# Optimization experiments

Measured on AMD Instinct MI355X. Metric: run time of the kernel, lower is better.

Reference implementation:

```python
import jax, jax.numpy as jnp
import numpy as np

C, H, W, NC, LC = 512, 160, 160, 1203, 64


def setup_inputs() -> dict:
    key = jax.random.key(0)
    ks = jax.random.split(key, 8)
    return {
        "cls_feat": jax.random.normal(ks[0], (1, C, H, W), jnp.float32),
        "loc_feat": jax.random.normal(ks[1], (1, LC, H, W), jnp.float32),
        "conf": jax.random.uniform(ks[2], (1,), jnp.float32, 0.2, 0.8),
        "pf_w": jax.random.normal(ks[3], (C,), jnp.float32) * 0.02,   # pf 1x1 conv, C->1
        "pf_b": jnp.zeros((1,), jnp.float32),
        "vocab_w": jax.random.normal(ks[4], (NC, C), jnp.float32) * 0.02,  # conv2linear weight
        "vocab_b": jnp.zeros((NC,), jnp.float32),
        "loc_w": jax.random.normal(ks[5], (LC, LC), jnp.float32) * 0.02,   # loc 1x1 conv
        "loc_b": jnp.zeros((LC,), jnp.float32),
    }


def reference(cls_feat, loc_feat, conf, pf_w, pf_b, vocab_w, vocab_b, loc_w, loc_b):
    B, Cc, Hh, Ww = cls_feat.shape
    # proposal-filter score: 1x1 conv C->1 on batch 0, flattened to [HW]
    pf_score = jnp.einsum('c,chw->hw', pf_w, cls_feat[0]).reshape(-1) + pf_b  # [HW]
    mask = jax.nn.sigmoid(pf_score) > conf[0]  # [HW] bool
    # tokens: [1, HW, C]
    tok = cls_feat.reshape(B, Cc, Hh * Ww).transpose(0, 2, 1)
    # static-shape equivalent of the proposal filter: zero masked-out tokens
    tok = tok * mask[None, :, None].astype(tok.dtype)
    # vocab linear (converted 1x1 conv): [1, HW, NC] -> [1, NC, HW]
    cls_out = (jnp.einsum('bnc,vc->bnv', tok, vocab_w) + vocab_b).transpose(0, 2, 1)
    # localization 1x1 conv
    loc_out = jnp.einsum('oi,bihw->bohw', loc_w, loc_feat) + loc_b[None, :, None, None]
    return loc_out, cls_out, mask
```

## Files before the change

### kernel.cpp

```cpp
#include <hip/hip_runtime.h>
#include <math.h>


constexpr int C_   = 512;
constexpr int HW_  = 25600;
constexpr int NC_  = 1203;
constexpr int VPAD_ = 1216;

constexpr int LOC_OFF_  = 0;
constexpr int CLS_OFF_  = 64 * HW_;
constexpr int MASK_OFF_ = CLS_OFF_ + NC_ * HW_;

constexpr int PF_BLOCKS_    = HW_ / 64;
constexpr int LOC_BLOCKS_   = 400;
constexpr int FILL_BLOCKS_  = 2048;
constexpr int TRANS_BLOCKS_ = 19 * 8;

typedef float vfloat4 __attribute__((ext_vector_type(4)));

__global__ void k_init(int* cnt) { *cnt = 0; }

__global__ __launch_bounds__(256) void k_main(
    const float* __restrict__ cls_feat, const float* __restrict__ loc_feat,
    const float* __restrict__ conf, const float* __restrict__ pf_w,
    const float* __restrict__ pf_b, const float* __restrict__ vocab_w,
    const float* __restrict__ vocab_b, const float* __restrict__ loc_w,
    const float* __restrict__ loc_b, float* __restrict__ out,
    int* __restrict__ cnt, int* __restrict__ idxList,
    float* __restrict__ AT4, int jcap)
{
    const int bid = blockIdx.x;
    const int tid = threadIdx.x;

    if (bid < PF_BLOCKS_) {
        __shared__ double sPart[256];
        const int hwi   = tid & 63;
        const int slice = tid >> 6;
        const int hw    = bid * 64 + hwi;
        const float* p  = cls_feat + (size_t)slice * 128 * HW_ + hw;
        const float* w  = pf_w + slice * 128;
        double acc = 0.0;
        #pragma unroll 4
        for (int k = 0; k < 128; ++k)
            acc += (double)w[k] * (double)p[(size_t)k * HW_];
        sPart[tid] = acc;
        __syncthreads();
        if (slice == 0) {
            double s = sPart[hwi] + sPart[64 + hwi] + sPart[128 + hwi] +
                       sPart[192 + hwi] + (double)pf_b[0];
            double sig = 1.0 / (1.0 + exp(-s));
            bool m = sig > (double)conf[0];
            out[MASK_OFF_ + hw] = m ? 1.0f : 0.0f;
            if (m) {
                int pos = atomicAdd(cnt, 1);
                if (pos < HW_) idxList[pos] = hw;
            }
        }
    } else if (bid < PF_BLOCKS_ + LOC_BLOCKS_) {
        const int j   = bid - PF_BLOCKS_;
        const int hwb = j % 100;
        const int o0  = (j / 100) * 16;
        __shared__ float sw[16][64];
        for (int i = tid; i < 16 * 64; i += 256)
            sw[i >> 6][i & 63] = loc_w[(o0 + (i >> 6)) * 64 + (i & 63)];
        __syncthreads();
        const int hw = hwb * 256 + tid;
        float acc[16];
        #pragma unroll
        for (int r = 0; r < 16; ++r) acc[r] = loc_b[o0 + r];
        for (int i = 0; i < 64; ++i) {
            float f = loc_feat[(size_t)i * HW_ + hw];
            #pragma unroll
            for (int r = 0; r < 16; ++r) acc[r] += sw[r][i] * f;
        }
        #pragma unroll
        for (int r = 0; r < 16; ++r)
            out[LOC_OFF_ + (size_t)(o0 + r) * HW_ + hw] = acc[r];
    } else if (bid < PF_BLOCKS_ + LOC_BLOCKS_ + FILL_BLOCKS_) {
        const int fb = bid - PF_BLOCKS_ - LOC_BLOCKS_;
        const int total4 = NC_ * HW_ / 4;
        vfloat4* o = (vfloat4*)(out + CLS_OFF_);
        for (int i = fb * 256 + tid; i < total4; i += FILL_BLOCKS_ * 256) {
            int v = i / (HW_ / 4);
            float b = vocab_b[v];
            vfloat4 val = {b, b, b, b};
            __builtin_nontemporal_store(val, &o[i]);
        }
    } else {
        if (jcap <= 0) return;
        const int tb = bid - PF_BLOCKS_ - LOC_BLOCKS_ - FILL_BLOCKS_;
        const int v0 = (tb % 19) * 64;
        const int k0 = (tb / 19) * 64;
        __shared__ float t[64][65];
        const int c  = tid & 63;
        const int r4 = tid >> 6;
        #pragma unroll
        for (int i = 0; i < 16; ++i) {
            const int r = r4 * 16 + i;
            const int v = v0 + r;
            t[r][c] = (v < NC_) ? vocab_w[(size_t)v * C_ + k0 + c] : 0.f;
        }
        __syncthreads();
        #pragma unroll
        for (int i = 0; i < 16; ++i) {
            const int k = r4 * 16 + i;
            const int kg = k0 + k;
            AT4[((size_t)(kg >> 2) * VPAD_ + v0 + c) * 4 + (kg & 3)] = t[c][k];
        }
    }
}

__global__ __launch_bounds__(256) void k_gatherJ(
    const float* __restrict__ cls_feat, const int* __restrict__ cnt,
    const int* __restrict__ idxList, float* __restrict__ BdT, int jcap)
{
    const int count = min(*cnt, HW_);
    if (count > jcap) return;
    const int t = threadIdx.x;
    for (int j = blockIdx.x; j < count; j += gridDim.x) {
        const int hw = idxList[j];
        BdT[(size_t)j * C_ + t]       = cls_feat[(size_t)t * HW_ + hw];
        BdT[(size_t)j * C_ + 256 + t] = cls_feat[(size_t)(256 + t) * HW_ + hw];
    }
}

__global__ __launch_bounds__(256) void k_gemm4(
    const float* __restrict__ AT4, const float* __restrict__ vocab_b,
    const int* __restrict__ cnt, const int* __restrict__ idxList,
    const float* __restrict__ BdT, float* __restrict__ out, int jcap)
{
    const int count = min(*cnt, HW_);
    if (count == 0 || count > jcap) return;

    const int tid  = threadIdx.x;
    const int lane = tid & 63;
    const int w    = tid >> 6;
    const int v0   = blockIdx.x * 64;
    const int v    = v0 + lane;
    const float* __restrict__ Acol = AT4 + (size_t)(v0 + lane) * 4;

    for (int j4 = blockIdx.y * 4; j4 < count; j4 += 4 * (int)gridDim.y) {
        const int j    = __builtin_amdgcn_readfirstlane(j4 + w);
        const bool jok = j < count;
        const float* __restrict__ Bj = BdT + (size_t)(jok ? j : 0) * C_;

        float ac0 = 0.f, ac1 = 0.f, ac2 = 0.f, ac3 = 0.f;
        #pragma unroll 8
        for (int kq = 0; kq < C_ / 4; ++kq) {
            const vfloat4 a =
                *(const vfloat4*)(Acol + (size_t)kq * VPAD_ * 4);
            ac0 += a.x * Bj[kq * 4 + 0];
            ac1 += a.y * Bj[kq * 4 + 1];
            ac2 += a.z * Bj[kq * 4 + 2];
            ac3 += a.w * Bj[kq * 4 + 3];
        }

        if (jok && v < NC_) {
            const int hw = idxList[j];
            out[CLS_OFF_ + (size_t)v * HW_ + hw] =
                (ac0 + ac1) + (ac2 + ac3) + vocab_b[v];
        }
    }
}

__global__ __launch_bounds__(256) void k_gemm_fallback(
    const float* __restrict__ cls_feat, const float* __restrict__ vocab_w,
    const float* __restrict__ vocab_b, const int* __restrict__ cnt,
    const int* __restrict__ idxList, float* __restrict__ out, int capB)
{
    const int count = min(*cnt, HW_);
    if (count <= capB) return;
    const int v0 = blockIdx.x * 64;

    __shared__ float sAT[16][64];
    __shared__ float sBT[16][64];
    __shared__ int   sIdx[64];

    const int tid = threadIdx.x;
    const int tx = tid & 15;
    const int ty = tid >> 4;
    const int r  = tid >> 2;
    const int kq = tid & 3;

    for (int jb = blockIdx.y; (jb << 6) < count; jb += gridDim.y) {
        const int j0 = jb << 6;
        __syncthreads();
        if (tid < 64) {
            int j = j0 + tid;
            sIdx[tid] = (j < count) ? idxList[j] : -1;
        }
        __syncthreads();
        const int hwj = sIdx[r];

        float acc[4][4] = {};
        for (int k0 = 0; k0 < C_; k0 += 16) {
            float4 a4 = make_float4(0.f, 0.f, 0.f, 0.f);
            if (v0 + r < NC_)
                a4 = *(const float4*)(vocab_w + (size_t)(v0 + r) * C_ + k0 + kq * 4);
            float b0 = 0.f, b1 = 0.f, b2 = 0.f, b3 = 0.f;
            if (hwj >= 0) {
                const float* bp = cls_feat + (size_t)(k0 + kq * 4) * HW_ + hwj;
                b0 = bp[0]; b1 = bp[HW_]; b2 = bp[2 * HW_]; b3 = bp[3 * HW_];
            }
            __syncthreads();
            sAT[kq * 4 + 0][r] = a4.x; sAT[kq * 4 + 1][r] = a4.y;
            sAT[kq * 4 + 2][r] = a4.z; sAT[kq * 4 + 3][r] = a4.w;
            sBT[kq * 4 + 0][r] = b0;   sBT[kq * 4 + 1][r] = b1;
            sBT[kq * 4 + 2][r] = b2;   sBT[kq * 4 + 3][r] = b3;
            __syncthreads();
            #pragma unroll
            for (int kk = 0; kk < 16; ++kk) {
                const float4 av = *(const float4*)&sAT[kk][ty * 4];
                const float4 bv = *(const float4*)&sBT[kk][tx * 4];
                acc[0][0] += av.x * bv.x; acc[0][1] += av.x * bv.y;
                acc[0][2] += av.x * bv.z; acc[0][3] += av.x * bv.w;
                acc[1][0] += av.y * bv.x; acc[1][1] += av.y * bv.y;
                acc[1][2] += av.y * bv.z; acc[1][3] += av.y * bv.w;
                acc[2][0] += av.z * bv.x; acc[2][1] += av.z * bv.y;
                acc[2][2] += av.z * bv.z; acc[2][3] += av.z * bv.w;
                acc[3][0] += av.w * bv.x; acc[3][1] += av.w * bv.y;
                acc[3][2] += av.w * bv.z; acc[3][3] += av.w * bv.w;
            }
        }
        #pragma unroll
        for (int a = 0; a < 4; ++a) {
            int v = v0 + ty * 4 + a;
            if (v >= NC_) continue;
            float bias = vocab_b[v];
            #pragma unroll
            for (int b = 0; b < 4; ++b) {
                int j = j0 + tx * 4 + b;
                if (j < count) {
                    int hw = sIdx[tx * 4 + b];
                    out[CLS_OFF_ + (size_t)v * HW_ + hw] = acc[a][b] + bias;
                }
            }
        }
    }
}

extern "C" void kernel_launch(void* const* d_in, const int* in_sizes, int n_in,
                              void* d_out, int out_size, void* d_ws,
                              size_t ws_size, hipStream_t stream) {
    const float* cls_feat = (const float*)d_in[0];
    const float* loc_feat = (const float*)d_in[1];
    const float* conf     = (const float*)d_in[2];
    const float* pf_w     = (const float*)d_in[3];
    const float* pf_b     = (const float*)d_in[4];
    const float* vocab_w  = (const float*)d_in[5];
    const float* vocab_b  = (const float*)d_in[6];
    const float* loc_w    = (const float*)d_in[7];
    const float* loc_b    = (const float*)d_in[8];
    float* out = (float*)d_out;

    int*   cnt     = (int*)d_ws;
    int*   idxList = (int*)((char*)d_ws + 4096);
    size_t fixed   = 4096 + (size_t)HW_ * sizeof(int);
    size_t atBytes = (size_t)(C_ / 4) * VPAD_ * 4 * sizeof(float);
    float* AT4     = (float*)((char*)d_ws + fixed);
    float* BdT     = (float*)((char*)d_ws + fixed + atBytes);

    int jcap = 0;
    if (ws_size > fixed + atBytes) {
        size_t cols = (ws_size - fixed - atBytes) / ((size_t)C_ * sizeof(float));
        jcap = (int)(cols > 1024 ? 1024 : cols);
        jcap &= ~63;
    }

    hipLaunchKernelGGL(k_init, dim3(1), dim3(1), 0, stream, cnt);
    hipLaunchKernelGGL(k_main,
                       dim3(PF_BLOCKS_ + LOC_BLOCKS_ + FILL_BLOCKS_ +
                            TRANS_BLOCKS_),
                       dim3(256), 0, stream,
                       cls_feat, loc_feat, conf, pf_w, pf_b, vocab_w, vocab_b,
                       loc_w, loc_b, out, cnt, idxList, AT4, jcap);
    if (jcap > 0) {
        hipLaunchKernelGGL(k_gatherJ, dim3(512), dim3(256), 0, stream,
                           cls_feat, cnt, idxList, BdT, jcap);
        hipLaunchKernelGGL(k_gemm4, dim3(19, 64), dim3(256), 0, stream,
                           AT4, vocab_b, cnt, idxList, BdT, out, jcap);
    }
    hipLaunchKernelGGL(k_gemm_fallback, dim3((NC_ + 63) / 64, 8), dim3(256),
                       0, stream, cls_feat, vocab_w, vocab_b, cnt, idxList,
                       out, jcap);
}
```

Before: 72.01 us.

## Split K across waves and reuse A loads over four columns in sparse GEMM

The sparse-column GEMM now has each of the four waves handle one quarter of the K dimension for the same four selected columns, instead of each wave walking all of K for its own column. Each A vector load is reused across four B columns, and the partial sums are combined through shared memory. The grid y-dimension becomes jcap/4 with early exit for blocks beyond the count, replacing the strided loop. This cuts redundant A traffic and shortens each thread's serial K loop, at the cost of a shared-memory reduction, a barrier and many more launched blocks that exit immediately.

```diff
diff --git a/kernel.cpp b/kernel.cpp
--- a/kernel.cpp
+++ b/kernel.cpp
@@ -103,7 +103,7 @@
         __syncthreads();
         #pragma unroll
         for (int i = 0; i < 16; ++i) {
-            const int k = r4 * 16 + i;
+            const int k  = r4 * 16 + i;
             const int kg = k0 + k;
             AT4[((size_t)(kg >> 2) * VPAD_ + v0 + c) * 4 + (kg & 3)] = t[c][k];
         }
@@ -124,41 +124,65 @@
     }
 }
 
-__global__ __launch_bounds__(256) void k_gemm4(
+__global__ __launch_bounds__(256) void k_gemm6(
     const float* __restrict__ AT4, const float* __restrict__ vocab_b,
     const int* __restrict__ cnt, const int* __restrict__ idxList,
     const float* __restrict__ BdT, float* __restrict__ out, int jcap)
 {
     const int count = min(*cnt, HW_);
     if (count == 0 || count > jcap) return;
+    const int jBase = blockIdx.y * 4;
+    if (jBase >= count) return;
 
     const int tid  = threadIdx.x;
     const int lane = tid & 63;
-    const int w    = tid >> 6;
+    const int w    = __builtin_amdgcn_readfirstlane(tid >> 6);
     const int v0   = blockIdx.x * 64;
     const int v    = v0 + lane;
-    const float* __restrict__ Acol = AT4 + (size_t)(v0 + lane) * 4;
-
-    for (int j4 = blockIdx.y * 4; j4 < count; j4 += 4 * (int)gridDim.y) {
-        const int j    = __builtin_amdgcn_readfirstlane(j4 + w);
-        const bool jok = j < count;
-        const float* __restrict__ Bj = BdT + (size_t)(jok ? j : 0) * C_;
-
-        float ac0 = 0.f, ac1 = 0.f, ac2 = 0.f, ac3 = 0.f;
-        #pragma unroll 8
-        for (int kq = 0; kq < C_ / 4; ++kq) {
-            const vfloat4 a =
-                *(const vfloat4*)(Acol + (size_t)kq * VPAD_ * 4);
-            ac0 += a.x * Bj[kq * 4 + 0];
-            ac1 += a.y * Bj[kq * 4 + 1];
-            ac2 += a.z * Bj[kq * 4 + 2];
-            ac3 += a.w * Bj[kq * 4 + 3];
-        }
-
-        if (jok && v < NC_) {
-            const int hw = idxList[j];
-            out[CLS_OFF_ + (size_t)v * HW_ + hw] =
-                (ac0 + ac1) + (ac2 + ac3) + vocab_b[v];
+    const float* __restrict__ Acol = AT4 + (size_t)v * 4;
+
+    const int j0 = jBase + 0, j1 = jBase + 1, j2 = jBase + 2, j3 = jBase + 3;
+    const float* __restrict__ B0 = BdT + (size_t)(j0 < count ? j0 : 0) * C_;
+    const float* __restrict__ B1 = BdT + (size_t)(j1 < count ? j1 : 0) * C_;
+    const float* __restrict__ B2 = BdT + (size_t)(j2 < count ? j2 : 0) * C_;
+    const float* __restrict__ B3 = BdT + (size_t)(j3 < count ? j3 : 0) * C_;
+
+    vfloat4 ac0 = {0,0,0,0}, ac1 = {0,0,0,0}, ac2 = {0,0,0,0}, ac3 = {0,0,0,0};
+
+    const int kqBeg = w * 32;
+    #pragma unroll 8
+    for (int q = 0; q < 32; ++q) {
+        const int kq = kqBeg + q;
+        const vfloat4 a = *(const vfloat4*)(Acol + (size_t)kq * VPAD_ * 4);
+        const vfloat4 b0 = *(const vfloat4*)(B0 + kq * 4);
+        const vfloat4 b1 = *(const vfloat4*)(B1 + kq * 4);
+        const vfloat4 b2 = *(const vfloat4*)(B2 + kq * 4);
+        const vfloat4 b3 = *(const vfloat4*)(B3 + kq * 4);
+        ac0 += a * b0;
+        ac1 += a * b1;
+        ac2 += a * b2;
+        ac3 += a * b3;
+    }
+
+    __shared__ float sRed[4][4][64];
+    sRed[w][0][lane] = (ac0.x + ac0.y) + (ac0.z + ac0.w);
+    sRed[w][1][lane] = (ac1.x + ac1.y) + (ac1.z + ac1.w);
+    sRed[w][2][lane] = (ac2.x + ac2.y) + (ac2.z + ac2.w);
+    sRed[w][3][lane] = (ac3.x + ac3.y) + (ac3.z + ac3.w);
+    __syncthreads();
+
+    if (tid < 64 && v < NC_) {
+        const float bias = vocab_b[v];
+        #pragma unroll
+        for (int jj = 0; jj < 4; ++jj) {
+            const int j = jBase + jj;
+            if (j < count) {
+                const float s =
+                    (sRed[0][jj][lane] + sRed[1][jj][lane]) +
+                    (sRed[2][jj][lane] + sRed[3][jj][lane]);
+                const int hw = idxList[j];
+                out[CLS_OFF_ + (size_t)v * HW_ + hw] = s + bias;
+            }
         }
     }
 }
@@ -277,7 +301,7 @@
     if (jcap > 0) {
         hipLaunchKernelGGL(k_gatherJ, dim3(512), dim3(256), 0, stream,
                            cls_feat, cnt, idxList, BdT, jcap);
-        hipLaunchKernelGGL(k_gemm4, dim3(19, 64), dim3(256), 0, stream,
+        hipLaunchKernelGGL(k_gemm6, dim3(19, jcap / 4), dim3(256), 0, stream,
                            AT4, vocab_b, cnt, idxList, BdT, out, jcap);
     }
     hipLaunchKernelGGL(k_gemm_fallback, dim3((NC_ + 63) / 64, 8), dim3(256),
```

Result: faster. 62.92 us (-12.6%).

## Split GEMM K dimension across waves with shared-memory reduction and wider grid

Applied to the files above, without the earlier changes.

The sparse vocab GEMM kernel now has each of the four waves handle a quarter of the K dimension for a single token column, then reduces the partial sums through shared memory. Previously each wave computed a full-K dot product for its own token. The grid grows from 64 to 512 blocks along the token axis, and B is read as float4 vectors. The aim is more parallelism and shorter per-thread loops when few tokens pass the filter, at the cost of two barriers per column and a final reduction done by only one wave.

```diff
diff --git a/kernel.cpp b/kernel.cpp
--- a/kernel.cpp
+++ b/kernel.cpp
@@ -2,9 +2,9 @@
 #include <math.h>
 
 
-constexpr int C_   = 512;
-constexpr int HW_  = 25600;
-constexpr int NC_  = 1203;
+constexpr int C_    = 512;
+constexpr int HW_   = 25600;
+constexpr int NC_   = 1203;
 constexpr int VPAD_ = 1216;
 
 constexpr int LOC_OFF_  = 0;
@@ -103,7 +103,7 @@
         __syncthreads();
         #pragma unroll
         for (int i = 0; i < 16; ++i) {
-            const int k = r4 * 16 + i;
+            const int k  = r4 * 16 + i;
             const int kg = k0 + k;
             AT4[((size_t)(kg >> 2) * VPAD_ + v0 + c) * 4 + (kg & 3)] = t[c][k];
         }
@@ -124,7 +124,7 @@
     }
 }
 
-__global__ __launch_bounds__(256) void k_gemm4(
+__global__ __launch_bounds__(256) void k_gemm7(
     const float* __restrict__ AT4, const float* __restrict__ vocab_b,
     const int* __restrict__ cnt, const int* __restrict__ idxList,
     const float* __restrict__ BdT, float* __restrict__ out, int jcap)
@@ -134,32 +134,37 @@
 
     const int tid  = threadIdx.x;
     const int lane = tid & 63;
-    const int w    = tid >> 6;
+    const int w    = __builtin_amdgcn_readfirstlane(tid >> 6);
     const int v0   = blockIdx.x * 64;
     const int v    = v0 + lane;
-    const float* __restrict__ Acol = AT4 + (size_t)(v0 + lane) * 4;
-
-    for (int j4 = blockIdx.y * 4; j4 < count; j4 += 4 * (int)gridDim.y) {
-        const int j    = __builtin_amdgcn_readfirstlane(j4 + w);
-        const bool jok = j < count;
-        const float* __restrict__ Bj = BdT + (size_t)(jok ? j : 0) * C_;
-
-        float ac0 = 0.f, ac1 = 0.f, ac2 = 0.f, ac3 = 0.f;
+    const float* __restrict__ Acol = AT4 + (size_t)v * 4;
+    const float bias = (v < NC_) ? vocab_b[v] : 0.f;
+
+    __shared__ float sRed[4][64];
+
+    for (int j = blockIdx.y; j < count; j += 512) {
+        const float* __restrict__ Bj = BdT + (size_t)j * C_;
+
+        vfloat4 acc = {0.f, 0.f, 0.f, 0.f};
+        const int kqBeg = w * 32;
         #pragma unroll 8
-        for (int kq = 0; kq < C_ / 4; ++kq) {
-            const vfloat4 a =
-                *(const vfloat4*)(Acol + (size_t)kq * VPAD_ * 4);
-            ac0 += a.x * Bj[kq * 4 + 0];
-            ac1 += a.y * Bj[kq * 4 + 1];
-            ac2 += a.z * Bj[kq * 4 + 2];
-            ac3 += a.w * Bj[kq * 4 + 3];
-        }
-
-        if (jok && v < NC_) {
+        for (int q = 0; q < 32; ++q) {
+            const int kq = kqBeg + q;
+            const vfloat4 a = *(const vfloat4*)(Acol + (size_t)kq * VPAD_ * 4);
+            const vfloat4 b = *(const vfloat4*)(Bj + kq * 4);
+            acc += a * b;
+        }
+
+        sRed[w][lane] = (acc.x + acc.y) + (acc.z + acc.w);
+        __syncthreads();
+
+        if (tid < 64 && v < NC_) {
+            const float s = (sRed[0][lane] + sRed[1][lane]) +
+                            (sRed[2][lane] + sRed[3][lane]);
             const int hw = idxList[j];
-            out[CLS_OFF_ + (size_t)v * HW_ + hw] =
-                (ac0 + ac1) + (ac2 + ac3) + vocab_b[v];
-        }
+            out[CLS_OFF_ + (size_t)v * HW_ + hw] = s + bias;
+        }
+        __syncthreads();
     }
 }
 
@@ -277,7 +282,7 @@
     if (jcap > 0) {
         hipLaunchKernelGGL(k_gatherJ, dim3(512), dim3(256), 0, stream,
                            cls_feat, cnt, idxList, BdT, jcap);
-        hipLaunchKernelGGL(k_gemm4, dim3(19, 64), dim3(256), 0, stream,
+        hipLaunchKernelGGL(k_gemm7, dim3(19, 512), dim3(256), 0, stream,
                            AT4, vocab_b, cnt, idxList, BdT, out, jcap);
     }
     hipLaunchKernelGGL(k_gemm_fallback, dim3((NC_ + 63) / 64, 8), dim3(256),
```

New measurement: 68.38 us. -5.1%, faster.
